# Performance work log

Hardware: AMD Instinct MI355X
Metric: run time of the kernel (lower is better)

## Reference

```python
import jax, jax.numpy as jnp
import numpy as np


def setup_inputs() -> dict:
    key = jax.random.key(0)
    ks = jax.random.split(key, 6)
    B, T, D, H = 32, 2048, 1024, 1024
    s = jax.random.normal(ks[0], (1, B, D), dtype=jnp.float32)
    h = jax.random.normal(ks[1], (B, T, D), dtype=jnp.float32)
    mask = jax.random.randint(ks[2], (B, T), 0, 2, dtype=jnp.int32)
    W = jax.random.normal(ks[3], (D, H), dtype=jnp.float32) * (6.0 / (D + H)) ** 0.5
    U = jax.random.normal(ks[4], (D, H), dtype=jnp.float32) * (6.0 / (D + H)) ** 0.5
    v = jax.random.normal(ks[5], (H, 1), dtype=jnp.float32) * (6.0 / (H + 1)) ** 0.5
    return {"s": s, "h": h, "mask": mask, "W": W, "U": U, "v": v}


def reference(s, h, mask, W, U, v):
    # mask-fill encoder states: zero out padded timesteps
    m = (mask != 0)[:, :, None]            # (B, T, 1)
    h = jnp.where(m, h, 0.0)               # (B, T, D)
    s_t = jnp.transpose(s, (1, 0, 2))      # (B, 1, D)
    proj_s = s_t @ W                       # (B, 1, H)
    proj_h = h @ U                         # (B, T, H)
    energy = jnp.tanh(proj_s + proj_h) @ v  # (B, T, 1)
    energy = jnp.where(m, energy, -1e9)
    score = jax.nn.softmax(energy, axis=1)  # softmax over time
    context = jnp.sum(score * h, axis=1)    # (B, D)
    return context
```

## Files before the change

kernel.cpp:

```cpp
#include <hip/hip_runtime.h>
#include <hip/hip_fp16.h>
#include <math.h>

#define BB 32
#define TT 2048
#define DD 1024
#define HH 1024
#define MM (BB*TT)

typedef _Float16 half8 __attribute__((ext_vector_type(8)));
typedef float f32x4 __attribute__((ext_vector_type(4)));

__device__ __forceinline__ float tanh_fast(float x) {
    float cx = fminf(fmaxf(x, -10.0f), 10.0f);
    float e2 = __expf(2.0f * cx);
    return (e2 - 1.0f) / (e2 + 1.0f);
}

__device__ __forceinline__ void load_lds16(const _Float16* g, _Float16* l) {
    __builtin_amdgcn_global_load_lds(
        (const __attribute__((address_space(1))) void*)g,
        (__attribute__((address_space(3))) void*)l, 16, 0, 0);
}

#define CAST_BLOCKS (MM/2)
#define UT_BLOCKS   1024
#define PS_BLOCKS   128
#define CPT_BLOCKS  32
#define TOTAL_SETUP (CAST_BLOCKS + UT_BLOCKS + PS_BLOCKS + CPT_BLOCKS)

__global__ __launch_bounds__(256)
void mega_setup_kernel(const float* __restrict__ h,
                       const int* __restrict__ mask,
                       _Float16* __restrict__ h16,
                       const float* __restrict__ U,
                       _Float16* __restrict__ Ut,
                       const float* __restrict__ s,
                       const float* __restrict__ W,
                       float* __restrict__ ps,
                       float* __restrict__ out,
                       int* __restrict__ rowlist,
                       int* __restrict__ cnts) {
    __shared__ float smem[1056];
    __shared__ int wsum[4];
    const int bid = blockIdx.x;
    const int tid = threadIdx.x;

    if (bid < CAST_BLOCKS) {
        const int row = bid * 2 + (tid >> 7);
        if (mask[row] == 0) return;
        const int c = (tid & 127) * 8;
        const long base = (long)row * DD + c;
        const float4 f0 = *(const float4*)(h + base);
        const float4 f1 = *(const float4*)(h + base + 4);
        half8 o;
        o[0] = (_Float16)f0.x; o[1] = (_Float16)f0.y;
        o[2] = (_Float16)f0.z; o[3] = (_Float16)f0.w;
        o[4] = (_Float16)f1.x; o[5] = (_Float16)f1.y;
        o[6] = (_Float16)f1.z; o[7] = (_Float16)f1.w;
        *(half8*)(h16 + base) = o;
        return;
    }

    if (bid < CAST_BLOCKS + UT_BLOCKS) {
        const int id = bid - CAST_BLOCKS;
        const int bx = id & 31, by = id >> 5;
        float (*tile)[33] = (float(*)[33])smem;
        const int tx = tid & 31, ty = tid >> 5;
#pragma unroll
        for (int j = 0; j < 4; ++j)
            tile[ty + j * 8][tx] = U[(long)(by * 32 + ty + j * 8) * HH + bx * 32 + tx];
        __syncthreads();
#pragma unroll
        for (int j = 0; j < 4; ++j)
            Ut[(long)(bx * 32 + ty + j * 8) * DD + by * 32 + tx] =
                (_Float16)tile[tx][ty + j * 8];
        return;
    }

    if (bid < CAST_BLOCKS + UT_BLOCKS + PS_BLOCKS) {
        const int id = bid - (CAST_BLOCKS + UT_BLOCKS);
        const int b = id & 31, nseg = id >> 5;
        const int n = nseg * 256 + tid;
        float* ss = smem;
#pragma unroll
        for (int j = 0; j < 4; ++j)
            ss[tid + j * 256] = s[b * DD + tid + j * 256];
        out[b * DD + n] = 0.0f;
        __syncthreads();
        float a[8];
#pragma unroll
        for (int j = 0; j < 8; ++j) a[j] = 0.f;
        for (int d = 0; d < DD; d += 8) {
#pragma unroll
            for (int j = 0; j < 8; ++j)
                a[j] += ss[d + j] * W[(long)(d + j) * HH + n];
        }
        ps[b * HH + n] = ((a[0]+a[1])+(a[2]+a[3])) + ((a[4]+a[5])+(a[6]+a[7]));
        return;
    }

    {
        const int b = bid - (CAST_BLOCKS + UT_BLOCKS + PS_BLOCKS);
        const int lane = tid & 63, w = tid >> 6;
        const int* mb = mask + b * TT;
        const int t0 = tid * 8;
        int m[8], c = 0;
#pragma unroll
        for (int j = 0; j < 8; ++j) { m[j] = (mb[t0 + j] != 0); c += m[j]; }
        int pref = c;
#pragma unroll
        for (int off = 1; off < 64; off <<= 1) {
            int nv = __shfl_up(pref, off, 64);
            if (lane >= off) pref += nv;
        }
        if (lane == 63) wsum[w] = pref;
        __syncthreads();
        int wbase = 0;
        for (int i = 0; i < w; ++i) wbase += wsum[i];
        int pos = wbase + pref - c;
#pragma unroll
        for (int j = 0; j < 8; ++j)
            if (m[j]) rowlist[b * TT + pos++] = t0 + j;
        const int total = wsum[0] + wsum[1] + wsum[2] + wsum[3];
        if (tid == 0) cnts[b] = total;
        __syncthreads();
        const int padded = ((total + 127) >> 7) << 7;
        const int lastt = (total > 0) ? rowlist[b * TT + total - 1] : 0;
        for (int ci = total + tid; ci < padded; ci += 256)
            rowlist[b * TT + ci] = lastt;
    }
}

#define Bb_K 32

__global__ __launch_bounds__(256)
void energy_gemm_kernel(const _Float16* __restrict__ h16,
                        const _Float16* __restrict__ Ut,
                        const float* __restrict__ ps,
                        const float* __restrict__ v,
                        const int* __restrict__ rowlist,
                        const int* __restrict__ cnts,
                        float* __restrict__ epart) {
    const int id = blockIdx.x;
    const int c  = id & 7;
    const int j  = id >> 3;
    const int nt = j & 7;
    const int mt = c + ((j >> 3) << 3);
    const int b   = mt >> 4;
    const int ci0 = (mt & 15) << 7;
    if (ci0 >= cnts[b]) return;

    __shared__ _Float16 AsF[2][4160];
    __shared__ _Float16 BsF[2][4160];
    __shared__ float ps_s[128];
    __shared__ float v_s[128];
    __shared__ int   rl[128];

    const int n0  = nt * 128;
    const int tid = threadIdx.x;
    const int wave = tid >> 6, lane = tid & 63;
    const int wm = wave >> 1, wn = wave & 1;

    if (tid < 128) {
        ps_s[tid] = ps[b * HH + n0 + tid];
        v_s[tid]  = v[n0 + tid];
        rl[tid]   = rowlist[b * TT + ci0 + tid];
    }
    __syncthreads();

    const int srow = wave * 32 + (lane >> 2);
    const int sseg = (lane & 3) * 8;
    const _Float16* gA0 = h16 + ((long)b * TT + rl[srow])      * DD + sseg;
    const _Float16* gA1 = h16 + ((long)b * TT + rl[srow + 16]) * DD + sseg;
    const _Float16* gB0 = Ut + (long)(n0 + srow) * DD + sseg;
    const _Float16* gB1 = gB0 + 16 * DD;

    f32x4 acc[4][4];
#pragma unroll
    for (int i = 0; i < 4; ++i)
#pragma unroll
        for (int j2 = 0; j2 < 4; ++j2) acc[i][j2] = (f32x4)0.0f;

    const int lk = (lane >> 4) * 8;
    const int lr = lane & 15;

    load_lds16(gA0, &AsF[0][(2 * wave) * 520]);
    load_lds16(gA1, &AsF[0][(2 * wave + 1) * 520]);
    load_lds16(gB0, &BsF[0][(2 * wave) * 520]);
    load_lds16(gB1, &BsF[0][(2 * wave + 1) * 520]);
    asm volatile("s_waitcnt vmcnt(0)" ::: "memory");
    __builtin_amdgcn_s_barrier();

#define KSTEP(CUR, NXT, KS)                                                   \
    {                                                                         \
        const int k1 = ((KS) + 1) * Bb_K;                                     \
        if (k1 < DD) {                                                        \
            load_lds16(gA0 + k1, &AsF[NXT][(2 * wave) * 520]);                \
            load_lds16(gA1 + k1, &AsF[NXT][(2 * wave + 1) * 520]);            \
            load_lds16(gB0 + k1, &BsF[NXT][(2 * wave) * 520]);                \
            load_lds16(gB1 + k1, &BsF[NXT][(2 * wave + 1) * 520]);            \
        }                                                                     \
        half8 af[4], bf[4];                                                   \
        _Pragma("unroll")                                                     \
        for (int tm = 0; tm < 4; ++tm)                                        \
            af[tm] = *(const half8*)&AsF[CUR][(wm * 64 + tm * 16 + lr) * 32 + \
                                             (wm * 4 + tm) * 8 + lk];         \
        _Pragma("unroll")                                                     \
        for (int tn = 0; tn < 4; ++tn)                                        \
            bf[tn] = *(const half8*)&BsF[CUR][(wn * 64 + tn * 16 + lr) * 32 + \
                                             (wn * 4 + tn) * 8 + lk];         \
        _Pragma("unroll")                                                     \
        for (int tm = 0; tm < 4; ++tm)                                        \
            _Pragma("unroll")                                                 \
            for (int tn = 0; tn < 4; ++tn)                                    \
                acc[tm][tn] = __builtin_amdgcn_mfma_f32_16x16x32_f16(         \
                    af[tm], bf[tn], acc[tm][tn], 0, 0, 0);                    \
        asm volatile("s_waitcnt vmcnt(0)" ::: "memory");                      \
        __builtin_amdgcn_s_barrier();                                         \
    }

#pragma unroll 1
    for (int ks = 0; ks < 32; ks += 2) {
        KSTEP(0, 1, ks);
        KSTEP(1, 0, ks + 1);
    }
#undef KSTEP

    float part[4][4];
#pragma unroll
    for (int tm = 0; tm < 4; ++tm) {
#pragma unroll
        for (int r = 0; r < 4; ++r) {
            float p = 0.f;
#pragma unroll
            for (int tn = 0; tn < 4; ++tn) {
                const int cl = wn * 64 + tn * 16 + lr;
                p += v_s[cl] * tanh_fast(acc[tm][tn][r] + ps_s[cl]);
            }
            part[tm][r] = p;
        }
    }
#pragma unroll
    for (int off = 1; off < 16; off <<= 1)
#pragma unroll
        for (int tm = 0; tm < 4; ++tm)
#pragma unroll
            for (int r = 0; r < 4; ++r)
                part[tm][r] += __shfl_xor(part[tm][r], off, 64);

    if ((lane & 15) == 0) {
        const int slot = nt * 2 + wn;
#pragma unroll
        for (int tm = 0; tm < 4; ++tm)
#pragma unroll
            for (int r = 0; r < 4; ++r) {
                const int ci = ci0 + wm * 64 + tm * 16 + (lane >> 4) * 4 + r;
                epart[(long)slot * MM + b * TT + ci] = part[tm][r];
            }
    }
}

__global__ void softmax_kernel(const float* __restrict__ epart,
                               const int* __restrict__ rowlist,
                               const int* __restrict__ cnts,
                               float* __restrict__ score) {
    const int b = blockIdx.x, tid = threadIdx.x;
    const int cnt = cnts[b];
    for (int t = tid; t < TT; t += 256) score[b * TT + t] = 0.0f;

    float e[8], mx = -1e30f;
#pragma unroll
    for (int i = 0; i < 8; ++i) {
        const int ci = i * 256 + tid;
        float sum = -1e30f;
        if (ci < cnt) {
            sum = 0.f;
#pragma unroll
            for (int p = 0; p < 16; ++p)
                sum += epart[(long)p * MM + b * TT + ci];
        }
        e[i] = sum;
        mx = fmaxf(mx, sum);
    }
#pragma unroll
    for (int off = 32; off > 0; off >>= 1) mx = fmaxf(mx, __shfl_xor(mx, off, 64));
    __shared__ float r4[4];
    if ((tid & 63) == 0) r4[tid >> 6] = mx;
    __syncthreads();
    mx = fmaxf(fmaxf(r4[0], r4[1]), fmaxf(r4[2], r4[3]));

    float tot = 0.f;
#pragma unroll
    for (int i = 0; i < 8; ++i) {
        const int ci = i * 256 + tid;
        e[i] = (ci < cnt) ? __expf(e[i] - mx) : 0.0f;
        tot += e[i];
    }
#pragma unroll
    for (int off = 32; off > 0; off >>= 1) tot += __shfl_xor(tot, off, 64);
    __shared__ float s4[4];
    if ((tid & 63) == 0) s4[tid >> 6] = tot;
    __syncthreads();
    tot = s4[0] + s4[1] + s4[2] + s4[3];
    const float inv = 1.0f / tot;
#pragma unroll
    for (int i = 0; i < 8; ++i) {
        const int ci = i * 256 + tid;
        if (ci < cnt)
            score[b * TT + rowlist[b * TT + ci]] = e[i] * inv;
    }
}

__global__ void context_kernel(const _Float16* __restrict__ h16,
                               const float* __restrict__ score,
                               float* __restrict__ out) {
    const int tc = blockIdx.x;
    const int b  = blockIdx.y;
    const int d0 = threadIdx.x * 8;
    float a[8];
#pragma unroll
    for (int j = 0; j < 8; ++j) a[j] = 0.f;
    for (int i = 0; i < 128; ++i) {
        const int t = tc * 128 + i;
        const float sc = score[(long)b * TT + t];
        if (sc != 0.0f) {
            const half8 hv = *(const half8*)(h16 + ((long)(b * TT + t)) * DD + d0);
#pragma unroll
            for (int j = 0; j < 8; ++j) a[j] += sc * (float)hv[j];
        }
    }
#pragma unroll
    for (int j = 0; j < 8; ++j) atomicAdd(&out[b * DD + d0 + j], a[j]);
}

extern "C" void kernel_launch(void* const* d_in, const int* in_sizes, int n_in,
                              void* d_out, int out_size, void* d_ws, size_t ws_size,
                              hipStream_t stream) {
    const float* s    = (const float*)d_in[0];
    const float* h    = (const float*)d_in[1];
    const int*   mask = (const int*)  d_in[2];
    const float* W    = (const float*)d_in[3];
    const float* U    = (const float*)d_in[4];
    const float* v    = (const float*)d_in[5];
    float* out = (float*)d_out;

    char* ws = (char*)d_ws;
    size_t off = 0;
    _Float16* h16 = (_Float16*)(ws + off); off += (size_t)MM * DD * 2;
    _Float16* Ut  = (_Float16*)(ws + off); off += (size_t)HH * DD * 2;
    float*    ps  = (float*)(ws + off);    off += (size_t)BB * HH * 4;
    float*    ep  = (float*)(ws + off);    off += (size_t)16 * MM * 4;
    float*    scr = (float*)(ws + off);    off += (size_t)MM * 4;
    int*      rlist = (int*)(ws + off);    off += (size_t)MM * 4;
    int*      cnts  = (int*)(ws + off);    off += 64 * 4;

    mega_setup_kernel<<<TOTAL_SETUP, 256, 0, stream>>>(h, mask, h16, U, Ut,
                                                       s, W, ps, out, rlist, cnts);
    energy_gemm_kernel<<<4096, 256, 0, stream>>>(h16, Ut, ps, v,
                                                 rlist, cnts, ep);
    softmax_kernel<<<BB, 256, 0, stream>>>(ep, rlist, cnts, scr);
    context_kernel<<<dim3(16, 32), 128, 0, stream>>>(h16, scr, out);
}
```

Before: 571.1 us.

## Triple-buffer LDS staging in energy GEMM with partial vmcnt waits

Replaces the double-buffered LDS pipeline with a three-stage ring, prefetching two K-steps ahead and waiting only until four loads remain outstanding. This lets global-to-LDS loads overlap more MFMA work instead of draining all loads each step. It also drops the padded, swizzled LDS layout for a plain [128][32] layout, which may introduce LDS bank conflicts on fragment reads, and it uses more LDS per block, which can lower occupancy.

New measurement: 566.0 us. About the same (-0.9%).

```diff
diff --git a/kernel.cpp b/kernel.cpp
--- a/kernel.cpp
+++ b/kernel.cpp
@@ -151,8 +151,8 @@
     const int ci0 = (mt & 15) << 7;
     if (ci0 >= cnts[b]) return;
 
-    __shared__ _Float16 AsF[2][4160];
-    __shared__ _Float16 BsF[2][4160];
+    __shared__ _Float16 As[3][128][32];
+    __shared__ _Float16 Bs[3][128][32];
     __shared__ float ps_s[128];
     __shared__ float v_s[128];
     __shared__ int   rl[128];
@@ -185,47 +185,63 @@
     const int lk = (lane >> 4) * 8;
     const int lr = lane & 15;
 
-    load_lds16(gA0, &AsF[0][(2 * wave) * 520]);
-    load_lds16(gA1, &AsF[0][(2 * wave + 1) * 520]);
-    load_lds16(gB0, &BsF[0][(2 * wave) * 520]);
-    load_lds16(gB1, &BsF[0][(2 * wave + 1) * 520]);
-    asm volatile("s_waitcnt vmcnt(0)" ::: "memory");
-    __builtin_amdgcn_s_barrier();
-
-#define KSTEP(CUR, NXT, KS)                                                   \
-    {                                                                         \
-        const int k1 = ((KS) + 1) * Bb_K;                                     \
-        if (k1 < DD) {                                                        \
-            load_lds16(gA0 + k1, &AsF[NXT][(2 * wave) * 520]);                \
-            load_lds16(gA1 + k1, &AsF[NXT][(2 * wave + 1) * 520]);            \
-            load_lds16(gB0 + k1, &BsF[NXT][(2 * wave) * 520]);                \
-            load_lds16(gB1 + k1, &BsF[NXT][(2 * wave + 1) * 520]);            \
-        }                                                                     \
-        half8 af[4], bf[4];                                                   \
-        _Pragma("unroll")                                                     \
-        for (int tm = 0; tm < 4; ++tm)                                        \
-            af[tm] = *(const half8*)&AsF[CUR][(wm * 64 + tm * 16 + lr) * 32 + \
-                                             (wm * 4 + tm) * 8 + lk];         \
+#define STAGE(BUF, KOFF)                                                      \
+    load_lds16(gA0 + (KOFF), &As[BUF][wave * 32][0]);                         \
+    load_lds16(gA1 + (KOFF), &As[BUF][wave * 32 + 16][0]);                    \
+    load_lds16(gB0 + (KOFF), &Bs[BUF][wave * 32][0]);                         \
+    load_lds16(gB1 + (KOFF), &Bs[BUF][wave * 32 + 16][0]);
+
+#define RDFRAG(CUR)                                                           \
+    half8 af[4], bf[4];                                                       \
+    _Pragma("unroll")                                                         \
+    for (int tm = 0; tm < 4; ++tm)                                            \
+        af[tm] = *(const half8*)&As[CUR][wm * 64 + tm * 16 + lr][lk];         \
+    _Pragma("unroll")                                                         \
+    for (int tn = 0; tn < 4; ++tn)                                            \
+        bf[tn] = *(const half8*)&Bs[CUR][wn * 64 + tn * 16 + lr][lk];
+
+#define DOMFMA                                                                \
+    _Pragma("unroll")                                                         \
+    for (int tm = 0; tm < 4; ++tm)                                            \
         _Pragma("unroll")                                                     \
         for (int tn = 0; tn < 4; ++tn)                                        \
-            bf[tn] = *(const half8*)&BsF[CUR][(wn * 64 + tn * 16 + lr) * 32 + \
-                                             (wn * 4 + tn) * 8 + lk];         \
-        _Pragma("unroll")                                                     \
-        for (int tm = 0; tm < 4; ++tm)                                        \
-            _Pragma("unroll")                                                 \
-            for (int tn = 0; tn < 4; ++tn)                                    \
-                acc[tm][tn] = __builtin_amdgcn_mfma_f32_16x16x32_f16(         \
-                    af[tm], bf[tn], acc[tm][tn], 0, 0, 0);                    \
-        asm volatile("s_waitcnt vmcnt(0)" ::: "memory");                      \
+            acc[tm][tn] = __builtin_amdgcn_mfma_f32_16x16x32_f16(             \
+                af[tm], bf[tn], acc[tm][tn], 0, 0, 0);
+
+#define KSTEP(CUR, STG, KS)                                                   \
+    {                                                                         \
+        RDFRAG(CUR)                                                           \
+        STAGE(STG, ((KS) + 2) * Bb_K)                                         \
+        DOMFMA                                                                \
+        asm volatile("s_waitcnt vmcnt(4)" ::: "memory");                      \
         __builtin_amdgcn_s_barrier();                                         \
     }
 
+    STAGE(0, 0)
+    STAGE(1, Bb_K)
+    asm volatile("s_waitcnt vmcnt(4)" ::: "memory");
+    __builtin_amdgcn_s_barrier();
+
 #pragma unroll 1
-    for (int ks = 0; ks < 32; ks += 2) {
-        KSTEP(0, 1, ks);
-        KSTEP(1, 0, ks + 1);
+    for (int ks = 0; ks < 30; ks += 3) {
+        KSTEP(0, 2, ks)
+        KSTEP(1, 0, ks + 1)
+        KSTEP(2, 1, ks + 2)
+    }
+    {
+        RDFRAG(0)
+        DOMFMA
+        asm volatile("s_waitcnt vmcnt(0)" ::: "memory");
+        __builtin_amdgcn_s_barrier();
+    }
+    {
+        RDFRAG(1)
+        DOMFMA
     }
 #undef KSTEP
+#undef DOMFMA
+#undef RDFRAG
+#undef STAGE
 
     float part[4][4];
 #pragma unroll
```
